# Performance work log

Measured on AMD Instinct MI355X. Metric: run time of the kernel, lower is better.

The kernel has to match this reference:

```python
import jax, jax.numpy as jnp
import numpy as np
from jax import lax

B, T, I, H, L = 64, 512, 256, 512, 2


def setup_inputs() -> dict:
    key = jax.random.key(0)
    ks = jax.random.split(key, 5)
    s_in = (6.0 / (H + I)) ** 0.5   # xavier-uniform-like scale
    s_hh = (6.0 / (H + H)) ** 0.5
    return {
        "x": jax.random.normal(ks[0], (B, T, I), jnp.float32),
        "h_0": jnp.zeros((L, B, H), jnp.float32),
        "W_ih_0": jax.random.normal(ks[1], (H, I), jnp.float32) * s_in,
        "W_hh_0": jax.random.normal(ks[2], (H, H), jnp.float32) * s_hh,
        "b_ih_0": jnp.zeros((H,), jnp.float32),
        "b_hh_0": jnp.zeros((H,), jnp.float32),
        "W_ih_1": jax.random.normal(ks[3], (H, H), jnp.float32) * s_hh,
        "W_hh_1": jax.random.normal(ks[4], (H, H), jnp.float32) * s_hh,
        "b_ih_1": jnp.zeros((H,), jnp.float32),
        "b_hh_1": jnp.zeros((H,), jnp.float32),
    }


def _rnn_layer(xs, h0, W_ih, W_hh, b_ih, b_hh):
    # Precompute the input-to-hidden projection for all timesteps at once
    # (same math as per-step F.linear, just batched): [B,T,H]
    xW = jnp.einsum('bti,hi->bth', xs, W_ih) + b_ih + b_hh

    def step(h, xw_t):  # h:[B,H], xw_t:[B,H]
        h_new = jnp.tanh(xw_t + h @ W_hh.T)
        return h_new, h_new

    h_last, ys = lax.scan(step, h0, jnp.swapaxes(xW, 0, 1))  # ys: [T,B,H]
    return jnp.swapaxes(ys, 0, 1), h_last


def reference(x, h_0, W_ih_0, W_hh_0, b_ih_0, b_hh_0,
              W_ih_1, W_hh_1, b_ih_1, b_hh_1):
    out0, h_n0 = _rnn_layer(x, h_0[0], W_ih_0, W_hh_0, b_ih_0, b_hh_0)
    out1, h_n1 = _rnn_layer(out0, h_0[1], W_ih_1, W_hh_1, b_ih_1, b_hh_1)
    h_n = jnp.stack([h_n0, h_n1], axis=0)  # [L,B,H]
    return out1, h_n
```

## Files before the change

kernel.cpp:

```cpp
#include <hip/hip_runtime.h>


#define kB 64
#define kT 512
#define kI 256
#define kH 512
#define kBH (kB * kH)

typedef _Float16 half8 __attribute__((ext_vector_type(8)));
typedef _Float16 half4v __attribute__((ext_vector_type(4)));
typedef float floatx4 __attribute__((ext_vector_type(4)));

constexpr size_t X16_B   = 0;
constexpr size_t OUT0M_B = 16u * 1024 * 1024;
constexpr size_t H1M_B   = OUT0M_B + (size_t)(kT + 1) * kBH * 2;
constexpr size_t CNT_B   = H1M_B + (size_t)(kT + 1) * kBH * 2;

__device__ inline half8 cvt8(const float* p) {
    const float4* p4 = (const float4*)p;
    float4 a = p4[0], b = p4[1];
    half8 h;
    h[0] = (_Float16)a.x; h[1] = (_Float16)a.y; h[2] = (_Float16)a.z; h[3] = (_Float16)a.w;
    h[4] = (_Float16)b.x; h[5] = (_Float16)b.y; h[6] = (_Float16)b.z; h[7] = (_Float16)b.w;
    return h;
}

__device__ inline void sc_store_half(_Float16* p, _Float16 v) {
    unsigned short u = __builtin_bit_cast(unsigned short, v);
    __hip_atomic_store((unsigned short*)p, u, __ATOMIC_RELAXED, __HIP_MEMORY_SCOPE_AGENT);
}

__device__ inline void wait_slots(const int* slots, int target) {
    const int* p = slots + (threadIdx.x & 31);
    int guard = 0;
    for (;;) {
        int v = __hip_atomic_load(p, __ATOMIC_RELAXED, __HIP_MEMORY_SCOPE_AGENT);
        if (__all(v >= target)) break;
        if (++guard > 50000000) break;
    }
    asm volatile("" ::: "memory");
}

__device__ inline void publish_block(int* slot, int t1, int tid) {
    asm volatile("" ::: "memory");
    __builtin_amdgcn_s_waitcnt(0x0F70);
    __syncthreads();
    if (tid == 0)
        __hip_atomic_store(slot, t1, __ATOMIC_RELAXED, __HIP_MEMORY_SCOPE_AGENT);
}

__global__ void cvt_x_kernel(const float* __restrict__ x, _Float16* __restrict__ x16) {
    size_t i = ((size_t)blockIdx.x * blockDim.x + threadIdx.x) * 4;
    size_t stride = (size_t)gridDim.x * blockDim.x * 4;
    const size_t n = (size_t)kB * kT * kI;
    for (; i < n; i += stride) {
        float4 v = *(const float4*)(x + i);
        half4v h;
        h[0] = (_Float16)v.x; h[1] = (_Float16)v.y; h[2] = (_Float16)v.z; h[3] = (_Float16)v.w;
        *(half4v*)(x16 + i) = h;
    }
}

__global__ void setup_kernel(const float* __restrict__ h0, _Float16* __restrict__ out0m,
                             _Float16* __restrict__ h1m, int* __restrict__ cnt) {
    int idx = blockIdx.x * blockDim.x + threadIdx.x;
    if (idx < kBH) out0m[idx] = (_Float16)h0[idx];
    else h1m[idx - kBH] = (_Float16)h0[idx];
    if (idx < 256) cnt[idx] = 0;
}

__global__ __launch_bounds__(256, 1) void scan_kernel(
    const _Float16* __restrict__ x16, _Float16* __restrict__ out0m,
    _Float16* __restrict__ h1m, int* __restrict__ slots0, int* __restrict__ slots1,
    float* __restrict__ out1,
    const float* __restrict__ wih0, const float* __restrict__ whh0,
    const float* __restrict__ bih0, const float* __restrict__ bhh0,
    const float* __restrict__ wih1, const float* __restrict__ whh1,
    const float* __restrict__ bih1, const float* __restrict__ bhh1) {
    __shared__ float lds[2][4][256];

    const int blk = blockIdx.x;
    const int tid = threadIdx.x;
    const int wave = tid >> 6;
    const int lane = tid & 63;
    const int r = lane & 15;
    const int q = lane >> 4;
    const int layer = blk >> 7;
    const int lb = blk & 127;
    const int g = lb >> 5;
    const int ct = lb & 31;
    const int c0 = ct * 16;
    const int b0 = g * 16;

    const int col = lane & 15;
    const int row = wave * 4 + (lane >> 4);
    const int cc = c0 + col;
    const int bb = b0 + row;
    const int roff = (wave * 16 + col) * 4 + (lane >> 4);

    if (layer == 0) {
        half8 wfi[2], wfh[4];
#pragma unroll
        for (int m = 0; m < 2; ++m)
            wfi[m] = cvt8(wih0 + (size_t)(c0 + r) * kI + wave * 64 + m * 32 + q * 8);
#pragma unroll
        for (int m = 0; m < 4; ++m)
            wfh[m] = cvt8(whh0 + (size_t)(c0 + r) * kH + wave * 128 + m * 32 + q * 8);
        const float bias = bih0[cc] + bhh0[cc];
        int* gslots = slots0 + g * 32;

        for (int t = 0; t < kT; ++t) {
            const _Float16* xrow = x16 + ((size_t)(b0 + r) * kT + t) * kI + wave * 64 + q * 8;
            half8 xa0 = *(const half8*)(xrow);
            half8 xa1 = *(const half8*)(xrow + 32);
            floatx4 a0 = {0.f, 0.f, 0.f, 0.f};
            floatx4 a1 = {0.f, 0.f, 0.f, 0.f};
            a0 = __builtin_amdgcn_mfma_f32_16x16x32_f16(xa0, wfi[0], a0, 0, 0, 0);
            a1 = __builtin_amdgcn_mfma_f32_16x16x32_f16(xa1, wfi[1], a1, 0, 0, 0);

            if (t > 0) wait_slots(gslots, t);
            const _Float16* hrow = out0m + (size_t)t * kBH + (size_t)(b0 + r) * kH
                                   + wave * 128 + q * 8;
            half8 h0v = *(const half8*)(hrow);
            half8 h1v = *(const half8*)(hrow + 32);
            half8 h2v = *(const half8*)(hrow + 64);
            half8 h3v = *(const half8*)(hrow + 96);
            a0 = __builtin_amdgcn_mfma_f32_16x16x32_f16(h0v, wfh[0], a0, 0, 0, 0);
            a1 = __builtin_amdgcn_mfma_f32_16x16x32_f16(h1v, wfh[1], a1, 0, 0, 0);
            a0 = __builtin_amdgcn_mfma_f32_16x16x32_f16(h2v, wfh[2], a0, 0, 0, 0);
            a1 = __builtin_amdgcn_mfma_f32_16x16x32_f16(h3v, wfh[3], a1, 0, 0, 0);

            *(floatx4*)(&lds[t & 1][wave][lane * 4]) = a0 + a1;
            __syncthreads();
            const float* lp = &lds[t & 1][0][0];
            float s = lp[roff] + lp[256 + roff] + lp[512 + roff] + lp[768 + roff];
            float v = tanhf(s + bias);
            sc_store_half(out0m + (size_t)(t + 1) * kBH + (size_t)bb * kH + cc, (_Float16)v);
            publish_block(&gslots[ct], t + 1, tid);
        }
    } else {
        half8 wfi[4], wfh[4];
#pragma unroll
        for (int m = 0; m < 4; ++m)
            wfi[m] = cvt8(wih1 + (size_t)(c0 + r) * kH + wave * 128 + m * 32 + q * 8);
#pragma unroll
        for (int m = 0; m < 4; ++m)
            wfh[m] = cvt8(whh1 + (size_t)(c0 + r) * kH + wave * 128 + m * 32 + q * 8);
        const float bias = bih1[cc] + bhh1[cc];
        int* g0slots = slots0 + g * 32;
        int* g1slots = slots1 + g * 32;

        for (int t = 0; t < kT; ++t) {
            floatx4 a0 = {0.f, 0.f, 0.f, 0.f};
            floatx4 a1 = {0.f, 0.f, 0.f, 0.f};
            if (t > 0) wait_slots(g1slots, t);
            const _Float16* hrow = h1m + (size_t)t * kBH + (size_t)(b0 + r) * kH
                                   + wave * 128 + q * 8;
            half8 h0v = *(const half8*)(hrow);
            half8 h1v = *(const half8*)(hrow + 32);
            half8 h2v = *(const half8*)(hrow + 64);
            half8 h3v = *(const half8*)(hrow + 96);
            a0 = __builtin_amdgcn_mfma_f32_16x16x32_f16(h0v, wfh[0], a0, 0, 0, 0);
            a1 = __builtin_amdgcn_mfma_f32_16x16x32_f16(h1v, wfh[1], a1, 0, 0, 0);
            a0 = __builtin_amdgcn_mfma_f32_16x16x32_f16(h2v, wfh[2], a0, 0, 0, 0);
            a1 = __builtin_amdgcn_mfma_f32_16x16x32_f16(h3v, wfh[3], a1, 0, 0, 0);
            wait_slots(g0slots, t + 1);
            const _Float16* irow = out0m + (size_t)(t + 1) * kBH + (size_t)(b0 + r) * kH
                                   + wave * 128 + q * 8;
            half8 i0 = *(const half8*)(irow);
            half8 i1 = *(const half8*)(irow + 32);
            half8 i2 = *(const half8*)(irow + 64);
            half8 i3 = *(const half8*)(irow + 96);
            a0 = __builtin_amdgcn_mfma_f32_16x16x32_f16(i0, wfi[0], a0, 0, 0, 0);
            a1 = __builtin_amdgcn_mfma_f32_16x16x32_f16(i1, wfi[1], a1, 0, 0, 0);
            a0 = __builtin_amdgcn_mfma_f32_16x16x32_f16(i2, wfi[2], a0, 0, 0, 0);
            a1 = __builtin_amdgcn_mfma_f32_16x16x32_f16(i3, wfi[3], a1, 0, 0, 0);

            *(floatx4*)(&lds[t & 1][wave][lane * 4]) = a0 + a1;
            __syncthreads();
            const float* lp = &lds[t & 1][0][0];
            float s = lp[roff] + lp[256 + roff] + lp[512 + roff] + lp[768 + roff];
            float v = tanhf(s + bias);
            out1[((size_t)bb * kT + t) * kH + cc] = v;
            sc_store_half(h1m + (size_t)(t + 1) * kBH + (size_t)bb * kH + cc, (_Float16)v);
            publish_block(&g1slots[ct], t + 1, tid);
        }
    }
}

__global__ void finalize_kernel(const _Float16* __restrict__ out0m,
                                const _Float16* __restrict__ h1m,
                                float* __restrict__ out) {
    int idx = blockIdx.x * blockDim.x + threadIdx.x;
    float* hn = out + (size_t)kB * kT * kH;
    if (idx < kBH) hn[idx] = (float)out0m[(size_t)kT * kBH + idx];
    else hn[idx] = (float)h1m[(size_t)kT * kBH + (idx - kBH)];
}

extern "C" void kernel_launch(void* const* d_in, const int* in_sizes, int n_in,
                              void* d_out, int out_size, void* d_ws, size_t ws_size,
                              hipStream_t stream) {
    const float* x    = (const float*)d_in[0];
    const float* h0in = (const float*)d_in[1];
    const float* wih0 = (const float*)d_in[2];
    const float* whh0 = (const float*)d_in[3];
    const float* bih0 = (const float*)d_in[4];
    const float* bhh0 = (const float*)d_in[5];
    const float* wih1 = (const float*)d_in[6];
    const float* whh1 = (const float*)d_in[7];
    const float* bih1 = (const float*)d_in[8];
    const float* bhh1 = (const float*)d_in[9];
    float* out = (float*)d_out;
    char* ws = (char*)d_ws;

    _Float16* x16   = (_Float16*)(ws + X16_B);
    _Float16* out0m = (_Float16*)(ws + OUT0M_B);
    _Float16* h1m   = (_Float16*)(ws + H1M_B);
    int* cnt        = (int*)(ws + CNT_B);
    int* slots0 = cnt;
    int* slots1 = cnt + 128;

    cvt_x_kernel<<<1024, 256, 0, stream>>>(x, x16);
    setup_kernel<<<(2 * kBH) / 256, 256, 0, stream>>>(h0in, out0m, h1m, cnt);
    scan_kernel<<<256, 256, 0, stream>>>(x16, out0m, h1m, slots0, slots1, out,
                                         wih0, whh0, bih0, bhh0, wih1, whh1, bih1, bhh1);
    finalize_kernel<<<(2 * kBH) / 256, 256, 0, stream>>>(out0m, h1m, out);
}
```

Measured before the change: 2.017 ms.

## Precompute layer-0 input projection and repartition scan into 24 wide workgroups

Moves the layer-0 input projection out of the recurrent loop into a separate MFMA GEMM kernel. It writes the projection into the output buffer as scratch, which layer 1 later overwrites. The scan now runs on 24 blocks of 1024 threads instead of 256 blocks of 256. Each block stages the hidden state into swizzled LDS and holds full K-length weight fragments in registers, and layer-1 blocks split recurrent and input products across wave pairs. The aim is fewer cross-block flag waits per step (each block waits on 1-3 peers instead of 32) and less per-step latency, in exchange for fewer active CUs and more MFMA work per block.

```diff
diff --git a/kernel.cpp b/kernel.cpp
--- a/kernel.cpp
+++ b/kernel.cpp
@@ -8,10 +8,9 @@
 #define kBH (kB * kH)
 
 typedef _Float16 half8 __attribute__((ext_vector_type(8)));
-typedef _Float16 half4v __attribute__((ext_vector_type(4)));
 typedef float floatx4 __attribute__((ext_vector_type(4)));
 
-constexpr size_t X16_B   = 0;
+constexpr size_t W16_B   = 0;
 constexpr size_t OUT0M_B = 16u * 1024 * 1024;
 constexpr size_t H1M_B   = OUT0M_B + (size_t)(kT + 1) * kBH * 2;
 constexpr size_t CNT_B   = H1M_B + (size_t)(kT + 1) * kBH * 2;
@@ -30,160 +29,189 @@
     __hip_atomic_store((unsigned short*)p, u, __ATOMIC_RELAXED, __HIP_MEMORY_SCOPE_AGENT);
 }
 
-__device__ inline void wait_slots(const int* slots, int target) {
-    const int* p = slots + (threadIdx.x & 31);
+__device__ inline void wait_slot(const int* p, int target) {
+    int guard = 0;
+    while (__hip_atomic_load(p, __ATOMIC_RELAXED, __HIP_MEMORY_SCOPE_AGENT) < target)
+        if (++guard > 100000000) break;
+    asm volatile("" ::: "memory");
+}
+
+__device__ inline void wait_pair(const int* slots, int target) {
+    const int* p = slots + (threadIdx.x & 1);
     int guard = 0;
     for (;;) {
         int v = __hip_atomic_load(p, __ATOMIC_RELAXED, __HIP_MEMORY_SCOPE_AGENT);
         if (__all(v >= target)) break;
-        if (++guard > 50000000) break;
+        if (++guard > 100000000) break;
     }
     asm volatile("" ::: "memory");
 }
 
-__device__ inline void publish_block(int* slot, int t1, int tid) {
+__device__ inline void wait_quarters(const int* slots, int own, int target) {
+    const int idx = threadIdx.x & 3;
+    const int* p = slots + idx;
+    int guard = 0;
+    for (;;) {
+        int v = (idx == own) ? target
+              : __hip_atomic_load(p, __ATOMIC_RELAXED, __HIP_MEMORY_SCOPE_AGENT);
+        if (__all(v >= target)) break;
+        if (++guard > 100000000) break;
+    }
     asm volatile("" ::: "memory");
-    __builtin_amdgcn_s_waitcnt(0x0F70);
-    __syncthreads();
-    if (tid == 0)
-        __hip_atomic_store(slot, t1, __ATOMIC_RELAXED, __HIP_MEMORY_SCOPE_AGENT);
-}
-
-__global__ void cvt_x_kernel(const float* __restrict__ x, _Float16* __restrict__ x16) {
-    size_t i = ((size_t)blockIdx.x * blockDim.x + threadIdx.x) * 4;
-    size_t stride = (size_t)gridDim.x * blockDim.x * 4;
-    const size_t n = (size_t)kB * kT * kI;
-    for (; i < n; i += stride) {
-        float4 v = *(const float4*)(x + i);
-        half4v h;
-        h[0] = (_Float16)v.x; h[1] = (_Float16)v.y; h[2] = (_Float16)v.z; h[3] = (_Float16)v.w;
-        *(half4v*)(x16 + i) = h;
-    }
-}
-
-__global__ void setup_kernel(const float* __restrict__ h0, _Float16* __restrict__ out0m,
-                             _Float16* __restrict__ h1m, int* __restrict__ cnt) {
+}
+
+__global__ void setup_kernel(const float* __restrict__ h0, const float* __restrict__ wih0,
+                             _Float16* __restrict__ out0m, _Float16* __restrict__ h1m,
+                             _Float16* __restrict__ w16, int* __restrict__ cnt) {
     int idx = blockIdx.x * blockDim.x + threadIdx.x;
     if (idx < kBH) out0m[idx] = (_Float16)h0[idx];
-    else h1m[idx - kBH] = (_Float16)h0[idx];
+    else if (idx < 2 * kBH) h1m[idx - kBH] = (_Float16)h0[idx];
+    w16[idx] = (_Float16)wih0[idx];
     if (idx < 256) cnt[idx] = 0;
 }
 
-__global__ __launch_bounds__(256, 1) void scan_kernel(
-    const _Float16* __restrict__ x16, _Float16* __restrict__ out0m,
-    _Float16* __restrict__ h1m, int* __restrict__ slots0, int* __restrict__ slots1,
-    float* __restrict__ out1,
-    const float* __restrict__ wih0, const float* __restrict__ whh0,
-    const float* __restrict__ bih0, const float* __restrict__ bhh0,
+__global__ __launch_bounds__(256) void xw_kernel(
+    const float* __restrict__ x, const _Float16* __restrict__ w16,
+    const float* __restrict__ bih, const float* __restrict__ bhh, float* xw) {
+    const int mb = blockIdx.x >> 3, nb = blockIdx.x & 7;
+    const int wave = threadIdx.x >> 6, lane = threadIdx.x & 63;
+    const int r = lane & 15, q = lane >> 4;
+    const int m0 = mb * 64 + wave * 16;
+    half8 a[8];
+#pragma unroll
+    for (int ko = 0; ko < 8; ++ko)
+        a[ko] = cvt8(x + (size_t)(m0 + r) * kI + ko * 32 + q * 8);
+#pragma unroll
+    for (int ct = 0; ct < 4; ++ct) {
+        const int cc = nb * 64 + ct * 16 + r;
+        const float bias = bih[cc] + bhh[cc];
+        floatx4 acc = {bias, bias, bias, bias};
+#pragma unroll
+        for (int ko = 0; ko < 8; ++ko) {
+            half8 b = *(const half8*)(w16 + (size_t)cc * kI + ko * 32 + q * 8);
+            acc = __builtin_amdgcn_mfma_f32_16x16x32_f16(a[ko], b, acc, 0, 0, 0);
+        }
+#pragma unroll
+        for (int j = 0; j < 4; ++j)
+            xw[(size_t)(m0 + q * 4 + j) * kH + cc] = acc[j];
+    }
+}
+
+__global__ __launch_bounds__(1024) void scan_kernel(
+    const float* xw,
+    _Float16* __restrict__ out0m, _Float16* __restrict__ h1m,
+    int* __restrict__ slots0, int* __restrict__ slots1,
+    float* out1,
+    const float* __restrict__ whh0,
     const float* __restrict__ wih1, const float* __restrict__ whh1,
     const float* __restrict__ bih1, const float* __restrict__ bhh1) {
-    __shared__ float lds[2][4][256];
+    __shared__ __align__(16) char smem[40960];
 
     const int blk = blockIdx.x;
     const int tid = threadIdx.x;
-    const int wave = tid >> 6;
-    const int lane = tid & 63;
-    const int r = lane & 15;
-    const int q = lane >> 4;
-    const int layer = blk >> 7;
-    const int lb = blk & 127;
-    const int g = lb >> 5;
-    const int ct = lb & 31;
-    const int c0 = ct * 16;
-    const int b0 = g * 16;
-
-    const int col = lane & 15;
-    const int row = wave * 4 + (lane >> 4);
-    const int cc = c0 + col;
-    const int bb = b0 + row;
-    const int roff = (wave * 16 + col) * 4 + (lane >> 4);
-
-    if (layer == 0) {
-        half8 wfi[2], wfh[4];
-#pragma unroll
-        for (int m = 0; m < 2; ++m)
-            wfi[m] = cvt8(wih0 + (size_t)(c0 + r) * kI + wave * 64 + m * 32 + q * 8);
-#pragma unroll
-        for (int m = 0; m < 4; ++m)
-            wfh[m] = cvt8(whh0 + (size_t)(c0 + r) * kH + wave * 128 + m * 32 + q * 8);
-        const float bias = bih0[cc] + bhh0[cc];
-        int* gslots = slots0 + g * 32;
+    const int wave = tid >> 6, lane = tid & 63;
+    const int r = lane & 15, q = lane >> 4;
+    const int rb = (r << 10), swz = (r & 7) << 4;
+
+    if (blk < 8) {
+        const int g = blk >> 1, half = blk & 1;
+        const int b0 = g * 16;
+        const int cc = half * 256 + wave * 16 + r;
+        half8 wfh[16];
+#pragma unroll
+        for (int ks = 0; ks < 16; ++ks)
+            wfh[ks] = cvt8(whh0 + (size_t)cc * kH + ks * 32 + q * 8);
+        int* myslot = slots0 + g * 2 + half;
+        const int* peerslot = slots0 + g * 2 + (half ^ 1);
+        const int srow = tid >> 6, sunit = tid & 63;
+        const size_t sg_off = (size_t)(b0 + srow) * kH + sunit * 8;
+        char* sdst = smem + (((srow << 10) | (sunit << 4)) ^ ((srow & 7) << 4));
 
         for (int t = 0; t < kT; ++t) {
-            const _Float16* xrow = x16 + ((size_t)(b0 + r) * kT + t) * kI + wave * 64 + q * 8;
-            half8 xa0 = *(const half8*)(xrow);
-            half8 xa1 = *(const half8*)(xrow + 32);
-            floatx4 a0 = {0.f, 0.f, 0.f, 0.f};
-            floatx4 a1 = {0.f, 0.f, 0.f, 0.f};
-            a0 = __builtin_amdgcn_mfma_f32_16x16x32_f16(xa0, wfi[0], a0, 0, 0, 0);
-            a1 = __builtin_amdgcn_mfma_f32_16x16x32_f16(xa1, wfi[1], a1, 0, 0, 0);
-
-            if (t > 0) wait_slots(gslots, t);
-            const _Float16* hrow = out0m + (size_t)t * kBH + (size_t)(b0 + r) * kH
-                                   + wave * 128 + q * 8;
-            half8 h0v = *(const half8*)(hrow);
-            half8 h1v = *(const half8*)(hrow + 32);
-            half8 h2v = *(const half8*)(hrow + 64);
-            half8 h3v = *(const half8*)(hrow + 96);
-            a0 = __builtin_amdgcn_mfma_f32_16x16x32_f16(h0v, wfh[0], a0, 0, 0, 0);
-            a1 = __builtin_amdgcn_mfma_f32_16x16x32_f16(h1v, wfh[1], a1, 0, 0, 0);
-            a0 = __builtin_amdgcn_mfma_f32_16x16x32_f16(h2v, wfh[2], a0, 0, 0, 0);
-            a1 = __builtin_amdgcn_mfma_f32_16x16x32_f16(h3v, wfh[3], a1, 0, 0, 0);
-
-            *(floatx4*)(&lds[t & 1][wave][lane * 4]) = a0 + a1;
-            __syncthreads();
-            const float* lp = &lds[t & 1][0][0];
-            float s = lp[roff] + lp[256 + roff] + lp[512 + roff] + lp[768 + roff];
-            float v = tanhf(s + bias);
-            sc_store_half(out0m + (size_t)(t + 1) * kBH + (size_t)bb * kH + cc, (_Float16)v);
-            publish_block(&gslots[ct], t + 1, tid);
+            float xwv[4];
+#pragma unroll
+            for (int j = 0; j < 4; ++j)
+                xwv[j] = xw[((size_t)(b0 + q * 4 + j) * kT + t) * kH + cc];
+            if (t > 0) wait_slot(peerslot, t);
+            *(half8*)sdst = *(const half8*)(out0m + (size_t)t * kBH + sg_off);
+            __syncthreads();
+            floatx4 acc = {0.f, 0.f, 0.f, 0.f};
+#pragma unroll
+            for (int ks = 0; ks < 16; ++ks) {
+                half8 la = *(const half8*)(smem + ((rb | (ks << 6) | (q << 4)) ^ swz));
+                acc = __builtin_amdgcn_mfma_f32_16x16x32_f16(la, wfh[ks], acc, 0, 0, 0);
+            }
+            _Float16* dst = out0m + (size_t)(t + 1) * kBH + (size_t)(b0 + q * 4) * kH + cc;
+#pragma unroll
+            for (int j = 0; j < 4; ++j)
+                sc_store_half(dst + (size_t)j * kH, (_Float16)tanhf(acc[j] + xwv[j]));
+            asm volatile("" ::: "memory");
+            __builtin_amdgcn_s_waitcnt(0x0F70);
+            __syncthreads();
+            if (tid == 0)
+                __hip_atomic_store(myslot, t + 1, __ATOMIC_RELAXED, __HIP_MEMORY_SCOPE_AGENT);
         }
     } else {
-        half8 wfi[4], wfh[4];
-#pragma unroll
-        for (int m = 0; m < 4; ++m)
-            wfi[m] = cvt8(wih1 + (size_t)(c0 + r) * kH + wave * 128 + m * 32 + q * 8);
-#pragma unroll
-        for (int m = 0; m < 4; ++m)
-            wfh[m] = cvt8(whh1 + (size_t)(c0 + r) * kH + wave * 128 + m * 32 + q * 8);
-        const float bias = bih1[cc] + bhh1[cc];
-        int* g0slots = slots0 + g * 32;
-        int* g1slots = slots1 + g * 32;
+        const int b2 = blk - 8;
+        const int g = b2 >> 2, qb = b2 & 3;
+        const int b0 = g * 16;
+        const int ct = wave >> 1, part = wave & 1;
+        const int cc = qb * 128 + ct * 16 + r;
+        half8 wf[16];
+        const float* wsrc = part ? wih1 : whh1;
+#pragma unroll
+        for (int ks = 0; ks < 16; ++ks)
+            wf[ks] = cvt8(wsrc + (size_t)cc * kH + ks * 32 + q * 8);
+        const float bias = (part == 0) ? (bih1[cc] + bhh1[cc]) : 0.f;
+        int* myslot = slots1 + g * 4 + qb;
+        const int* gq = slots1 + g * 4;
+        const int* gh = slots0 + g * 2;
+        const int u = ct * 64 + lane;
+        const int srow = u >> 5, sunit = u & 31;
+        const size_t sg_off = (size_t)(b0 + srow) * kH + sunit * 16;
+        const int tbase = part ? 16384 : 0;
+        char* sd0 = smem + tbase + ((((srow << 10) | (sunit << 5))) ^ ((srow & 7) << 4));
+        char* sd1 = smem + tbase + ((((srow << 10) | (sunit << 5)) | 16) ^ ((srow & 7) << 4));
+        float* redp = (float*)(smem + 32768) + (ct * 256 + lane * 4);
 
         for (int t = 0; t < kT; ++t) {
-            floatx4 a0 = {0.f, 0.f, 0.f, 0.f};
-            floatx4 a1 = {0.f, 0.f, 0.f, 0.f};
-            if (t > 0) wait_slots(g1slots, t);
-            const _Float16* hrow = h1m + (size_t)t * kBH + (size_t)(b0 + r) * kH
-                                   + wave * 128 + q * 8;
-            half8 h0v = *(const half8*)(hrow);
-            half8 h1v = *(const half8*)(hrow + 32);
-            half8 h2v = *(const half8*)(hrow + 64);
-            half8 h3v = *(const half8*)(hrow + 96);
-            a0 = __builtin_amdgcn_mfma_f32_16x16x32_f16(h0v, wfh[0], a0, 0, 0, 0);
-            a1 = __builtin_amdgcn_mfma_f32_16x16x32_f16(h1v, wfh[1], a1, 0, 0, 0);
-            a0 = __builtin_amdgcn_mfma_f32_16x16x32_f16(h2v, wfh[2], a0, 0, 0, 0);
-            a1 = __builtin_amdgcn_mfma_f32_16x16x32_f16(h3v, wfh[3], a1, 0, 0, 0);
-            wait_slots(g0slots, t + 1);
-            const _Float16* irow = out0m + (size_t)(t + 1) * kBH + (size_t)(b0 + r) * kH
-                                   + wave * 128 + q * 8;
-            half8 i0 = *(const half8*)(irow);
-            half8 i1 = *(const half8*)(irow + 32);
-            half8 i2 = *(const half8*)(irow + 64);
-            half8 i3 = *(const half8*)(irow + 96);
-            a0 = __builtin_amdgcn_mfma_f32_16x16x32_f16(i0, wfi[0], a0, 0, 0, 0);
-            a1 = __builtin_amdgcn_mfma_f32_16x16x32_f16(i1, wfi[1], a1, 0, 0, 0);
-            a0 = __builtin_amdgcn_mfma_f32_16x16x32_f16(i2, wfi[2], a0, 0, 0, 0);
-            a1 = __builtin_amdgcn_mfma_f32_16x16x32_f16(i3, wfi[3], a1, 0, 0, 0);
-
-            *(floatx4*)(&lds[t & 1][wave][lane * 4]) = a0 + a1;
-            __syncthreads();
-            const float* lp = &lds[t & 1][0][0];
-            float s = lp[roff] + lp[256 + roff] + lp[512 + roff] + lp[768 + roff];
-            float v = tanhf(s + bias);
-            out1[((size_t)bb * kT + t) * kH + cc] = v;
-            sc_store_half(h1m + (size_t)(t + 1) * kBH + (size_t)bb * kH + cc, (_Float16)v);
-            publish_block(&g1slots[ct], t + 1, tid);
+            const _Float16* sl;
+            if (part == 0) {
+                if (t > 0) wait_quarters(gq, qb, t);
+                sl = h1m + (size_t)t * kBH;
+            } else {
+                wait_pair(gh, t + 1);
+                sl = out0m + (size_t)(t + 1) * kBH;
+            }
+            half8 s0 = *(const half8*)(sl + sg_off);
+            half8 s1 = *(const half8*)(sl + sg_off + 8);
+            *(half8*)sd0 = s0;
+            *(half8*)sd1 = s1;
+            __syncthreads();
+            floatx4 acc = {0.f, 0.f, 0.f, 0.f};
+            const char* tb = smem + tbase;
+#pragma unroll
+            for (int ks = 0; ks < 16; ++ks) {
+                half8 la = *(const half8*)(tb + ((rb | (ks << 6) | (q << 4)) ^ swz));
+                acc = __builtin_amdgcn_mfma_f32_16x16x32_f16(la, wf[ks], acc, 0, 0, 0);
+            }
+            if (part == 1) *(floatx4*)redp = acc;
+            __syncthreads();
+            if (part == 0) {
+                floatx4 o = *(const floatx4*)redp;
+#pragma unroll
+                for (int j = 0; j < 4; ++j) {
+                    float v = tanhf(acc[j] + o[j] + bias);
+                    out1[((size_t)(b0 + q * 4 + j) * kT + t) * kH + cc] = v;
+                    sc_store_half(h1m + (size_t)(t + 1) * kBH + (size_t)(b0 + q * 4 + j) * kH + cc,
+                                  (_Float16)v);
+                }
+            }
+            asm volatile("" ::: "memory");
+            __builtin_amdgcn_s_waitcnt(0x0F70);
+            __syncthreads();
+            if (tid == 0)
+                __hip_atomic_store(myslot, t + 1, __ATOMIC_RELAXED, __HIP_MEMORY_SCOPE_AGENT);
         }
     }
 }
@@ -213,16 +241,16 @@
     float* out = (float*)d_out;
     char* ws = (char*)d_ws;
 
-    _Float16* x16   = (_Float16*)(ws + X16_B);
+    _Float16* w16   = (_Float16*)(ws + W16_B);
     _Float16* out0m = (_Float16*)(ws + OUT0M_B);
     _Float16* h1m   = (_Float16*)(ws + H1M_B);
     int* cnt        = (int*)(ws + CNT_B);
     int* slots0 = cnt;
-    int* slots1 = cnt + 128;
-
-    cvt_x_kernel<<<1024, 256, 0, stream>>>(x, x16);
-    setup_kernel<<<(2 * kBH) / 256, 256, 0, stream>>>(h0in, out0m, h1m, cnt);
-    scan_kernel<<<256, 256, 0, stream>>>(x16, out0m, h1m, slots0, slots1, out,
-                                         wih0, whh0, bih0, bhh0, wih1, whh1, bih1, bhh1);
-    finalize_kernel<<<(2 * kBH) / 256, 256, 0, stream>>>(out0m, h1m, out);
-}
+    int* slots1 = cnt + 32;
+
+    setup_kernel<<<512, 256, 0, stream>>>(h0in, wih0, out0m, h1m, w16, cnt);
+    xw_kernel<<<4096, 256, 0, stream>>>(x, w16, bih0, bhh0, out);
+    scan_kernel<<<24, 1024, 0, stream>>>(out, out0m, h1m, slots0, slots1, out,
+                                         whh0, wih1, whh1, bih1, bhh1);
+    finalize_kernel<<<256, 256, 0, stream>>>(out0m, h1m, out);
+}
```

Result: no change. 2.046 ms (+1.5%).
